# Kernel tuning notes

Hardware: AMD Instinct MI355X
Metric: run time of the kernel (lower is better)

The kernel has to match this reference:

```python
import jax, jax.numpy as jnp
import numpy as np

HIDDEN = 4096
N_HEADS = 32
N_KV_HEADS = 8
HEAD_DIM = HIDDEN // N_HEADS  # 128
N_REP = N_HEADS // N_KV_HEADS  # 4
ROPE_THETA = 10000.0
B, S = 2, 2048


def setup_inputs() -> dict:
    key = jax.random.key(0)
    ks = jax.random.split(key, 9)
    sc = 1.0 / np.sqrt(HIDDEN)
    query = jax.random.normal(ks[0], (B, S, HIDDEN), jnp.float32)
    key_t = jax.random.normal(ks[1], (B, S, HIDDEN), jnp.float32)
    value = jax.random.normal(ks[2], (B, S, HIDDEN), jnp.float32)
    position_ids = jnp.sort(jax.random.randint(ks[3], (B, S), 0, S), axis=-1)
    Wq = jax.random.normal(ks[4], (HIDDEN, N_HEADS * HEAD_DIM), jnp.float32) * sc
    Wk = jax.random.normal(ks[5], (HIDDEN, N_KV_HEADS * HEAD_DIM), jnp.float32) * sc
    Wv = jax.random.normal(ks[6], (HIDDEN, N_KV_HEADS * HEAD_DIM), jnp.float32) * sc
    Wo = jax.random.normal(ks[7], (N_HEADS * HEAD_DIM, HIDDEN), jnp.float32) * sc
    return {"query": query, "key": key_t, "value": value,
            "position_ids": position_ids,
            "Wq": Wq, "Wk": Wk, "Wv": Wv, "Wo": Wo}


def _rotate_half(x):
    x1, x2 = jnp.split(x, 2, axis=-1)
    return jnp.concatenate((-x2, x1), axis=-1)


def _rope_cos_sin(position_ids):
    # inv_freq: [head_dim/2]
    inv_freq = 1.0 / (ROPE_THETA ** (jnp.arange(0, HEAD_DIM, 2, dtype=jnp.float32) / HEAD_DIM))
    # freqs: [B, S, head_dim/2] via per-position lookup (equiv. to cache gather cos_cached[position_ids])
    freqs = position_ids[..., None].astype(jnp.float32) * inv_freq
    emb = jnp.concatenate((freqs, freqs), axis=-1)          # [B, S, head_dim]
    return jnp.cos(emb)[:, None, :, :], jnp.sin(emb)[:, None, :, :]  # [B,1,S,hd]


def reference(query, key, value, position_ids, Wq, Wk, Wv, Wo):
    nb, q_len, _ = query.shape
    # QKV projections (bias-free linear)
    q = jnp.einsum('bse,ef->bsf', query, Wq).reshape(nb, q_len, N_HEADS, HEAD_DIM).transpose(0, 2, 1, 3)
    k = jnp.einsum('bse,ef->bsf', key, Wk).reshape(nb, q_len, N_KV_HEADS, HEAD_DIM).transpose(0, 2, 1, 3)
    v = jnp.einsum('bse,ef->bsf', value, Wv).reshape(nb, q_len, N_KV_HEADS, HEAD_DIM).transpose(0, 2, 1, 3)
    # RoPE
    cos, sin = _rope_cos_sin(position_ids)
    q = q * cos + _rotate_half(q) * sin
    k = k * cos + _rotate_half(k) * sin
    # GQA repeat_kv: [B, kvH, S, d] -> [B, H, S, d]
    k = jnp.repeat(k, N_REP, axis=1)
    v = jnp.repeat(v, N_REP, axis=1)
    # scaled dot-product attention (flash-attn semantics, no padding mask)
    scale = 1.0 / jnp.sqrt(jnp.asarray(HEAD_DIM, q.dtype))
    scores = jnp.einsum('bhqd,bhkd->bhqk', q, k) * scale
    probs = jax.nn.softmax(scores, axis=-1)
    ctx = jnp.einsum('bhqk,bhkd->bhqd', probs, v)
    ctx = ctx.transpose(0, 2, 1, 3).reshape(nb, q_len, N_HEADS * HEAD_DIM)
    return jnp.einsum('bsf,fe->bse', ctx, Wo)
```

## Files before the change

### kernel.cpp

```cpp
#include <hip/hip_runtime.h>
#include <hip/hip_bf16.h>

typedef __attribute__((ext_vector_type(8))) short bf16x8;
typedef __attribute__((ext_vector_type(4))) float f32x4;
typedef __attribute__((ext_vector_type(16))) float f32x16;
typedef __attribute__((ext_vector_type(2))) float f32x2;
typedef __attribute__((ext_vector_type(2))) unsigned uint2x;

#define AS1(p) ((const __attribute__((address_space(1))) void*)(p))
#define AS3(p) ((__attribute__((address_space(3))) void*)(p))

__device__ inline unsigned cvtpk_bf16(float lo, float hi) {
  unsigned r;
  asm("v_cvt_pk_bf16_f32 %0, %1, %2" : "=v"(r) : "v"(lo), "v"(hi));
  return r;
}

__device__ inline uint2x plswap(unsigned a, unsigned b) {
  return __builtin_amdgcn_permlane32_swap(a, b, false, false);
}

__device__ inline f32x2 pkadd(f32x2 a, f32x2 b) {
  f32x2 d;
  asm("v_pk_add_f32 %0, %1, %2" : "=v"(d) : "v"(a), "v"(b));
  return d;
}
__device__ inline f32x2 pkmul(f32x2 a, f32x2 b) {
  f32x2 d;
  asm("v_pk_mul_f32 %0, %1, %2" : "=v"(d) : "v"(a), "v"(b));
  return d;
}


__global__ __launch_bounds__(256) void xconv_kv(const float* __restrict__ k_in,
                                                const float* __restrict__ v_in,
                                                __hip_bfloat16* __restrict__ kc,
                                                __hip_bfloat16* __restrict__ vc) {
  const float* in = blockIdx.y ? v_in : k_in;
  __hip_bfloat16* out = blockIdx.y ? vc : kc;
  size_t i = ((size_t)blockIdx.x * 256 + threadIdx.x) * 4;
  float4 v = *(const float4*)(in + i);
  union { __hip_bfloat16 h[4]; ushort4 u; } o;
  o.h[0] = __float2bfloat16(v.x);
  o.h[1] = __float2bfloat16(v.y);
  o.h[2] = __float2bfloat16(v.z);
  o.h[3] = __float2bfloat16(v.w);
  *(ushort4*)(out + i) = o.u;
}

__global__ __launch_bounds__(256) void xconv(const float* __restrict__ in,
                                             __hip_bfloat16* __restrict__ out) {
  size_t i = ((size_t)blockIdx.x * 256 + threadIdx.x) * 4;
  float4 v = *(const float4*)(in + i);
  union { __hip_bfloat16 h[4]; ushort4 u; } o;
  o.h[0] = __float2bfloat16(v.x);
  o.h[1] = __float2bfloat16(v.y);
  o.h[2] = __float2bfloat16(v.z);
  o.h[3] = __float2bfloat16(v.w);
  *(ushort4*)(out + i) = o.u;
}

__global__ __launch_bounds__(256) void wtransAll(const float* __restrict__ Wq,
                                                 const float* __restrict__ Wo,
                                                 const float* __restrict__ Wk,
                                                 const float* __restrict__ Wv,
                                                 __hip_bfloat16* __restrict__ WqT,
                                                 __hip_bfloat16* __restrict__ WoT,
                                                 __hip_bfloat16* __restrict__ WkT,
                                                 __hip_bfloat16* __restrict__ WvT) {
  const int z = blockIdx.z;
  const int N = (z < 2) ? 4096 : 1024;
  const int n0 = blockIdx.x << 5;
  if (n0 >= N) return;
  const float* W = (z == 0) ? Wq : (z == 1) ? Wo : (z == 2) ? Wk : Wv;
  __hip_bfloat16* WT = (z == 0) ? WqT : (z == 1) ? WoT : (z == 2) ? WkT : WvT;
  __shared__ float t[32][33];
  const int k0 = blockIdx.y << 5;
  const int tx = threadIdx.x, ty = threadIdx.y;
#pragma unroll
  for (int j = 0; j < 4; ++j)
    t[ty + j * 8][tx] = W[(size_t)(k0 + ty + j * 8) * N + n0 + tx];
  __syncthreads();
#pragma unroll
  for (int j = 0; j < 4; ++j)
    WT[(size_t)(n0 + ty + j * 8) * 4096 + k0 + tx] = __float2bfloat16(t[tx][ty + j * 8]);
}

__global__ __launch_bounds__(256) void rope(__hip_bfloat16* __restrict__ X,
                                            const int* __restrict__ pos,
                                            int hbits, float scale) {
  const int t = blockIdx.x * 256 + threadIdx.x;
  const int j = t & 63;
  const int rest = t >> 6;
  const int h = rest & ((1 << hbits) - 1);
  const int row = rest >> hbits;
  const float p = (float)pos[row];
  const float fr = p * exp2f((float)j * -0.2076205059304601f);
  float sn, cs;
  __sincosf(fr, &sn, &cs);
  const size_t base = (((size_t)row << hbits) + h) * 128 + j;
  const float x0 = __bfloat162float(X[base]);
  const float x1 = __bfloat162float(X[base + 64]);
  X[base]      = __float2bfloat16((x0 * cs - x1 * sn) * scale);
  X[base + 64] = __float2bfloat16((x1 * cs + x0 * sn) * scale);
}

__global__ __launch_bounds__(256) void gemm_kv(const __hip_bfloat16* __restrict__ Ak,
                                               const __hip_bfloat16* __restrict__ Av,
                                               const __hip_bfloat16* __restrict__ BkT,
                                               const __hip_bfloat16* __restrict__ BvT,
                                               __hip_bfloat16* __restrict__ Kp,
                                               __hip_bfloat16* __restrict__ VT) {
  __shared__ __align__(16) __hip_bfloat16 sh[17408];
  __hip_bfloat16* As = sh;
  __hip_bfloat16* Bs = sh + 8192;
  const int zz = blockIdx.z;
  const __hip_bfloat16* A  = zz ? Av : Ak;
  const __hip_bfloat16* BT = zz ? BvT : BkT;
  const int K = 4096, N = 1024;
  const int tid = threadIdx.x;
  const int lane = tid & 63, w = tid >> 6;
  const int m0 = blockIdx.y * 128, n0 = blockIdx.x * 128;
  const int wr = (w >> 1) * 64, wc = (w & 1) * 64;
  const int l15 = lane & 15, lg = lane >> 4;

  f32x4 acc[4][4] = {};
  const int srow = lane >> 3;
  const int scol = (lane & 7) * 8;

  for (int k0 = 0; k0 < K; k0 += 64) {
    __syncthreads();
#pragma unroll
    for (int i = 0; i < 4; ++i) {
      const int chunk = i * 4 + w;
      const int row = chunk * 8 + srow;
      __builtin_amdgcn_global_load_lds(AS1(A + (size_t)(m0 + row) * K + k0 + scol),
                                       AS3(As + chunk * 512), 16, 0, 0);
      __builtin_amdgcn_global_load_lds(AS1(BT + (size_t)(n0 + row) * K + k0 + scol),
                                       AS3(Bs + chunk * 512), 16, 0, 0);
    }
    __syncthreads();
#pragma unroll
    for (int kk = 0; kk < 2; ++kk) {
      bf16x8 af[4], bfr[4];
#pragma unroll
      for (int r = 0; r < 4; ++r) {
        af[r]  = *(const bf16x8*)(As + (wr + r * 16 + l15) * 64 + kk * 32 + lg * 8);
        bfr[r] = *(const bf16x8*)(Bs + (wc + r * 16 + l15) * 64 + kk * 32 + lg * 8);
      }
#pragma unroll
      for (int r = 0; r < 4; ++r)
#pragma unroll
        for (int c = 0; c < 4; ++c)
          acc[r][c] = __builtin_amdgcn_mfma_f32_16x16x32_bf16(af[r], bfr[c], acc[r][c], 0, 0, 0);
    }
  }

  if (zz == 0) {
#pragma unroll
    for (int r = 0; r < 4; ++r)
#pragma unroll
      for (int c = 0; c < 4; ++c)
#pragma unroll
        for (int i = 0; i < 4; ++i)
          Kp[(size_t)(m0 + wr + r * 16 + lg * 4 + i) * N + n0 + wc + c * 16 + l15] =
              __float2bfloat16(acc[r][c][i]);
  } else {
    __syncthreads();
    __hip_bfloat16* T = sh;
#pragma unroll
    for (int r = 0; r < 4; ++r)
#pragma unroll
      for (int c = 0; c < 4; ++c) {
        const int col = wc + c * 16 + l15;
        const int row = wr + r * 16 + lg * 4;
        union { __hip_bfloat16 h[4]; unsigned long long u; } pkv;
#pragma unroll
        for (int i = 0; i < 4; ++i) pkv.h[i] = __float2bfloat16(acc[r][c][i]);
        *(unsigned long long*)(T + col * 136 + row) = pkv.u;
      }
    __syncthreads();
    const int b = m0 >> 11, s0g = m0 & 2047, g = n0 >> 7;
    __hip_bfloat16* Vh = VT + (size_t)(b * 8 + g) * 128 * 2048;
    const int chunk = tid & 15;
#pragma unroll
    for (int it = 0; it < 8; ++it) {
      const int d = it * 16 + (tid >> 4);
      bf16x8 vv = *(const bf16x8*)(T + d * 136 + chunk * 8);
      *(bf16x8*)(Vh + (size_t)d * 2048 + s0g + chunk * 8) = vv;
    }
  }
}


__device__ inline int tile_off(int row, int k) {
  return (((row >> 4) << 1) + (k >> 5)) * 512 + (row & 15) * 32 +
         ((k & 31) ^ ((row & 8) << 1));
}

__device__ inline void stageA(const __hip_bfloat16* __restrict__ src, int ld, int row0,
                              int kt, int h, __hip_bfloat16* ldsT, int w, int lane) {
#pragma unroll
  for (int li = 0; li < 2; ++li) {
    const int t = li * 8 + w;
    const int grp = ((t >> 3) << 1) + h;
    const int srl = (t & 7) >> 1, sk = t & 1;
    const int rowbase = grp * 64 + srl * 16;
    __hip_bfloat16* dst = ldsT + ((((rowbase >> 4) << 1) + sk) << 9);
    const int r = lane >> 2;
    const int ku = (lane & 3) ^ ((r & 8) >> 2);
    __builtin_amdgcn_global_load_lds(
        AS1(src + (size_t)(row0 + rowbase + r) * ld + kt + (sk << 5) + (ku << 3)),
        AS3(dst), 16, 0, 0);
  }
}

__device__ inline void stageB(const __hip_bfloat16* __restrict__ src, int ld, int col0,
                              int kt, int h, __hip_bfloat16* ldsT, int w, int lane) {
#pragma unroll
  for (int li = 0; li < 2; ++li) {
    const int t = li * 8 + w;
    const int q = t >> 2;
    const int srl = (t >> 1) & 1, sk = t & 1;
    const int colbase = q * 64 + h * 32 + srl * 16;
    __hip_bfloat16* dst = ldsT + ((((colbase >> 4) << 1) + sk) << 9);
    const int r = lane >> 2;
    const int ku = (lane & 3) ^ ((r & 8) >> 2);
    __builtin_amdgcn_global_load_lds(
        AS1(src + (size_t)(col0 + colbase + r) * ld + kt + (sk << 5) + (ku << 3)),
        AS3(dst), 16, 0, 0);
  }
}

template <int OUT_F32>
__global__ __launch_bounds__(512, 1) void gemm256(const __hip_bfloat16* __restrict__ A,
                                                  const __hip_bfloat16* __restrict__ BT,
                                                  void* __restrict__ Cout,
                                                  int M, int N, int K) {
  __shared__ __align__(16) __hip_bfloat16 lds[2][2][16384];
  const int tid = threadIdx.x;
  const int lane = tid & 63, w = tid >> 6;
  const int l15 = lane & 15, lg = lane >> 4;
  const int wm = w >> 2, wn = w & 3;
  const int nbx = N >> 8;
  const int nwg = (M >> 8) * nbx;
  const int bid = blockIdx.x;
  const int swz = (bid & 7) * (nwg >> 3) + (bid >> 3);
  const int m0 = (swz / nbx) << 8, n0 = (swz % nbx) << 8;

  f32x4 acc[8][4] = {};
  const int NT = K >> 6;

  stageA(A, K, m0, 0, 0, &lds[0][0][0], w, lane);
  stageB(BT, K, n0, 0, 0, &lds[0][1][0], w, lane);
  stageA(A, K, m0, 0, 1, &lds[0][0][0], w, lane);
  stageB(BT, K, n0, 0, 1, &lds[0][1][0], w, lane);
  stageA(A, K, m0, 64, 0, &lds[1][0][0], w, lane);
  stageB(BT, K, n0, 64, 0, &lds[1][1][0], w, lane);
  asm volatile("s_waitcnt vmcnt(4)" ::: "memory");
  __builtin_amdgcn_s_barrier();

  for (int j = 0; j < NT; ++j) {
    const int buf = j & 1;
    const __hip_bfloat16* Ab = &lds[buf][0][0];
    const __hip_bfloat16* Bb = &lds[buf][1][0];
    __hip_bfloat16* An = &lds[buf ^ 1][0][0];
    __hip_bfloat16* Bn = &lds[buf ^ 1][1][0];
    __hip_bfloat16* Ac = &lds[buf][0][0];
    __hip_bfloat16* Bc = &lds[buf][1][0];
    const int kt1 = (j + 1) << 6, kt2 = (j + 2) << 6;
    const bool s1 = (j + 1) < NT, s2 = (j + 2) < NT;

    auto phase = [&](int rq, int cq, int sid) {
      bf16x8 af[2][4], bfr[2][2];
#pragma unroll
      for (int kk = 0; kk < 2; ++kk) {
#pragma unroll
        for (int rf = 0; rf < 4; ++rf)
          af[kk][rf] = *(const bf16x8*)(Ab +
              tile_off(wm * 128 + (rq * 4 + rf) * 16 + l15, kk * 32 + lg * 8));
#pragma unroll
        for (int cf = 0; cf < 2; ++cf)
          bfr[kk][cf] = *(const bf16x8*)(Bb +
              tile_off(wn * 64 + (cq * 2 + cf) * 16 + l15, kk * 32 + lg * 8));
      }
      if (sid == 0)      { if (s1) stageA(A, K, m0, kt1, 1, An, w, lane); }
      else if (sid == 1) { if (s1) stageB(BT, K, n0, kt1, 1, Bn, w, lane); }
      else if (sid == 2) { if (s2) stageA(A, K, m0, kt2, 0, Ac, w, lane); }
      else {
        if (s2) stageB(BT, K, n0, kt2, 0, Bc, w, lane);
        if (s2) asm volatile("s_waitcnt vmcnt(4)" ::: "memory");
        else    asm volatile("s_waitcnt vmcnt(0)" ::: "memory");
      }
      __builtin_amdgcn_s_barrier();
      asm volatile("s_waitcnt lgkmcnt(0)" ::: "memory");
      __builtin_amdgcn_sched_barrier(0);
      __builtin_amdgcn_s_setprio(1);
#pragma unroll
      for (int kk = 0; kk < 2; ++kk)
#pragma unroll
        for (int rf = 0; rf < 4; ++rf)
#pragma unroll
          for (int cf = 0; cf < 2; ++cf)
            acc[rq * 4 + rf][cq * 2 + cf] = __builtin_amdgcn_mfma_f32_16x16x32_bf16(
                af[kk][rf], bfr[kk][cf], acc[rq * 4 + rf][cq * 2 + cf], 0, 0, 0);
      __builtin_amdgcn_s_setprio(0);
      __builtin_amdgcn_s_barrier();
    };
    phase(0, 0, 0);
    phase(0, 1, 1);
    phase(1, 0, 2);
    phase(1, 1, 3);
  }

#pragma unroll
  for (int rf = 0; rf < 8; ++rf)
#pragma unroll
    for (int cf = 0; cf < 4; ++cf)
#pragma unroll
      for (int i = 0; i < 4; ++i) {
        const size_t row = (size_t)(m0 + wm * 128 + rf * 16 + lg * 4 + i);
        const size_t col = (size_t)(n0 + wn * 64 + cf * 16 + l15);
        if (OUT_F32)
          ((float*)Cout)[row * N + col] = acc[rf][cf][i];
        else
          ((__hip_bfloat16*)Cout)[row * N + col] = __float2bfloat16(acc[rf][cf][i]);
      }
}

__global__ __launch_bounds__(512) void attn(const __hip_bfloat16* __restrict__ Q,
                                            const __hip_bfloat16* __restrict__ Kp,
                                            const __hip_bfloat16* __restrict__ VT,
                                            const int* __restrict__ pos,
                                            __hip_bfloat16* __restrict__ ctx,
                                            float qs) {
  const int tid = threadIdx.x;
  const int lane = tid & 63, w = tid >> 6;
  const int l31 = lane & 31, hi = lane >> 5;
  const int qt = blockIdx.x, h = blockIdx.y, b = blockIdx.z;
  const int kvh = h >> 2;
  const int q0 = qt * 256 + w * 32;

  const __hip_bfloat16* Qh = Q + (size_t)(b * 2048) * 4096 + h * 128;
  const __hip_bfloat16* Kh = Kp + (size_t)(b * 2048) * 1024 + kvh * 128;
  const __hip_bfloat16* Vh = VT + (size_t)(b * 8 + kvh) * 128 * 2048;

  __shared__ __hip_bfloat16 Ks[2][64 * 128];
  __shared__ __hip_bfloat16 Vs[2][128 * 64];

  auto stage = [&](int buf, int s0) {
#pragma unroll
    for (int j = 0; j < 2; ++j) {
      const int idx = w * 64 + lane + j * 512;
      const int rK = idx >> 4, uK = idx & 15;
      __builtin_amdgcn_global_load_lds(
          AS1(Kh + (size_t)(s0 + rK) * 1024 + ((uK ^ (rK & 7)) << 3)),
          AS3(&Ks[buf][(w * 64 + j * 512) * 8]), 16, 0, 0);
      const int rV = idx >> 3, uV = idx & 7;
      __builtin_amdgcn_global_load_lds(
          AS1(Vh + (size_t)rV * 2048 + s0 + ((uV ^ (rV & 7)) << 3)),
          AS3(&Vs[buf][(w * 64 + j * 512) * 8]), 16, 0, 0);
    }
  };

  stage(0, 0);

  const int qrow = q0 + l31;
  const float pp = (float)pos[b * 2048 + qrow];
  bf16x8 qf[8];
  {
#pragma unroll
    for (int kd = 0; kd < 4; ++kd) {
      bf16x8 rlo = *(const bf16x8*)(Qh + (size_t)qrow * 4096 + kd * 16 + hi * 8);
      bf16x8 rhi = *(const bf16x8*)(Qh + (size_t)qrow * 4096 + (kd + 4) * 16 + hi * 8);
      bf16x8 olo, ohi;
#pragma unroll
      for (int e = 0; e < 8; ++e) {
        const int j = kd * 16 + hi * 8 + e;
        const float fr = pp * exp2f((float)j * -0.2076205059304601f);
        float sn, cs;
        __sincosf(fr, &sn, &cs);
        const float x0 = __uint_as_float(((unsigned)(unsigned short)rlo[e]) << 16);
        const float x1 = __uint_as_float(((unsigned)(unsigned short)rhi[e]) << 16);
        __hip_bfloat16 h0 = __float2bfloat16((x0 * cs - x1 * sn) * qs);
        __hip_bfloat16 h1 = __float2bfloat16((x1 * cs + x0 * sn) * qs);
        olo[e] = *(short*)&h0;
        ohi[e] = *(short*)&h1;
      }
      qf[kd] = olo;
      qf[kd + 4] = ohi;
    }
  }

  f32x16 o[4] = {};
  float m = -1e30f, lsum = 0.f;
  __syncthreads();

  auto tile = [&](int tt, int cur, bool pf) {
    if (pf) stage(cur ^ 1, (tt + 1) * 64);

    f32x16 p[2] = {};
    __builtin_amdgcn_s_setprio(1);
#pragma unroll
    for (int n = 0; n < 2; ++n)
#pragma unroll
      for (int kd = 0; kd < 8; ++kd) {
        const int row = n * 32 + l31;
        bf16x8 kf = *(const bf16x8*)(&Ks[cur][row * 128 + (((2 * kd + hi) ^ (row & 7)) << 3)]);
        p[n] = __builtin_amdgcn_mfma_f32_32x32x16_bf16(kf, qf[kd], p[n], 0, 0, 0);
      }
    __builtin_amdgcn_s_setprio(0);

    float t16[16];
#pragma unroll
    for (int e = 0; e < 16; ++e) t16[e] = fmaxf(p[0][e], p[1][e]);
    const float u0 = fmaxf(fmaxf(t16[0], t16[1]), t16[2]);
    const float u1 = fmaxf(fmaxf(t16[3], t16[4]), t16[5]);
    const float u2 = fmaxf(fmaxf(t16[6], t16[7]), t16[8]);
    const float u3 = fmaxf(fmaxf(t16[9], t16[10]), t16[11]);
    const float u4 = fmaxf(fmaxf(t16[12], t16[13]), t16[14]);
    float pmax = fmaxf(fmaxf(fmaxf(u0, u1), u2), fmaxf(fmaxf(u3, u4), t16[15]));
    {
      uint2x r = plswap(__float_as_uint(pmax), __float_as_uint(pmax));
      pmax = fmaxf(__uint_as_float(r[0]), __uint_as_float(r[1]));
    }
    if (!__all(pmax - m <= 8.0f)) {
      const float mnew = fmaxf(m, pmax);
      const float fac = exp2f(m - mnew);
      m = mnew;
      lsum *= fac;
      f32x2 f2; f2[0] = fac; f2[1] = fac;
#pragma unroll
      for (int dc = 0; dc < 4; ++dc)
#pragma unroll
        for (int i = 0; i < 8; ++i) {
          f32x2 a; a[0] = o[dc][2 * i]; a[1] = o[dc][2 * i + 1];
          a = pkmul(a, f2);
          o[dc][2 * i] = a[0]; o[dc][2 * i + 1] = a[1];
        }
    }
    f32x2 mneg; mneg[0] = -m; mneg[1] = -m;
#pragma unroll
    for (int n = 0; n < 2; ++n)
#pragma unroll
      for (int i = 0; i < 8; ++i) {
        f32x2 a; a[0] = p[n][2 * i]; a[1] = p[n][2 * i + 1];
        a = pkadd(a, mneg);
        p[n][2 * i] = exp2f(a[0]);
        p[n][2 * i + 1] = exp2f(a[1]);
      }
    f32x2 s[8];
#pragma unroll
    for (int i = 0; i < 8; ++i) {
      f32x2 a; a[0] = p[0][2 * i]; a[1] = p[0][2 * i + 1];
      f32x2 bb; bb[0] = p[1][2 * i]; bb[1] = p[1][2 * i + 1];
      s[i] = pkadd(a, bb);
    }
#pragma unroll
    for (int i = 0; i < 4; ++i) s[i] = pkadd(s[i], s[i + 4]);
    s[0] = pkadd(s[0], s[2]);
    s[1] = pkadd(s[1], s[3]);
    s[0] = pkadd(s[0], s[1]);
    float rs = s[0][0] + s[0][1];
    {
      uint2x r = plswap(__float_as_uint(rs), __float_as_uint(rs));
      rs = __uint_as_float(r[0]) + __uint_as_float(r[1]);
    }
    lsum += rs;

    __builtin_amdgcn_s_setprio(1);
#pragma unroll
    for (int n = 0; n < 2; ++n)
#pragma unroll
      for (int ks = 0; ks < 2; ++ks) {
        const int bse = ks * 8;
        unsigned a1 = cvtpk_bf16(p[n][bse + 0], p[n][bse + 1]);
        unsigned b1 = cvtpk_bf16(p[n][bse + 4], p[n][bse + 5]);
        unsigned a2 = cvtpk_bf16(p[n][bse + 2], p[n][bse + 3]);
        unsigned b2 = cvtpk_bf16(p[n][bse + 6], p[n][bse + 7]);
        uint2x s1 = plswap(a1, b1);
        uint2x s2 = plswap(a2, b2);
        union { unsigned u[4]; bf16x8 v; } pw = {{s1[0], s2[0], s1[1], s2[1]}};
        const int slot = n * 2 + ks;
#pragma unroll
        for (int dc = 0; dc < 4; ++dc) {
          const int row = dc * 32 + l31;
          bf16x8 vf = *(const bf16x8*)(&Vs[cur][row * 64 + (((2 * slot + hi) ^ (row & 7)) << 3)]);
          o[dc] = __builtin_amdgcn_mfma_f32_32x32x16_bf16(vf, pw.v, o[dc], 0, 0, 0);
        }
      }
    __builtin_amdgcn_s_setprio(0);
    __syncthreads();
  };

  for (int t2 = 0; t2 < 16; ++t2) {
    tile(2 * t2, 0, true);
    tile(2 * t2 + 1, 1, t2 < 15);
  }

  const float inv = 1.0f / lsum;
  const size_t rowbase = ((size_t)(b * 2048 + q0 + l31)) * 4096 + h * 128;
#pragma unroll
  for (int dc = 0; dc < 4; ++dc)
#pragma unroll
    for (int g = 0; g < 4; ++g) {
      union { unsigned short us[4]; ushort4 u4; } pk;
#pragma unroll
      for (int e = 0; e < 4; ++e) {
        __hip_bfloat16 hv = __float2bfloat16(o[dc][g * 4 + e] * inv);
        pk.us[e] = *(unsigned short*)&hv;
      }
      *(ushort4*)(ctx + rowbase + dc * 32 + g * 8 + hi * 4) = pk.u4;
    }
}


extern "C" void kernel_launch(void* const* d_in, const int* in_sizes, int n_in,
                              void* d_out, int out_size, void* d_ws, size_t ws_size,
                              hipStream_t stream) {
  const float* q_in = (const float*)d_in[0];
  const float* k_in = (const float*)d_in[1];
  const float* v_in = (const float*)d_in[2];
  const int* pos    = (const int*)d_in[3];
  const float* Wq   = (const float*)d_in[4];
  const float* Wk   = (const float*)d_in[5];
  const float* Wv   = (const float*)d_in[6];
  const float* Wo   = (const float*)d_in[7];

  char* ws = (char*)d_ws;
  __hip_bfloat16* xbuf = (__hip_bfloat16*)(ws);
  __hip_bfloat16* WqT  = (__hip_bfloat16*)(ws + 33554432);
  __hip_bfloat16* WkT  = (__hip_bfloat16*)(ws + 67108864);
  __hip_bfloat16* WvT  = (__hip_bfloat16*)(ws + 75497472);
  __hip_bfloat16* WoT  = (__hip_bfloat16*)(ws + 83886080);
  __hip_bfloat16* Qp   = (__hip_bfloat16*)(ws + 117440512);
  __hip_bfloat16* Kp   = (__hip_bfloat16*)(ws + 150994944);
  __hip_bfloat16* VTb  = (__hip_bfloat16*)(ws + 167772160);
  __hip_bfloat16* vconv = WqT;

  wtransAll<<<dim3(128, 128, 4), dim3(32, 8), 0, stream>>>(Wq, Wo, Wk, Wv,
                                                           WqT, WoT, WkT, WvT);
  xconv<<<16384, 256, 0, stream>>>(q_in, xbuf);
  gemm256<0><<<256, 512, 0, stream>>>(xbuf, WqT, Qp, 4096, 4096, 4096);
  xconv_kv<<<dim3(16384, 2), 256, 0, stream>>>(k_in, v_in, xbuf, vconv);
  gemm_kv<<<dim3(8, 32, 2), 256, 0, stream>>>(xbuf, vconv, WkT, WvT, Kp, VTb);
  rope<<<8192, 256, 0, stream>>>(Kp, pos, 3, 1.0f);
  attn<<<dim3(8, 32, 2), 512, 0, stream>>>(Qp, Kp, VTb, pos, xbuf,
                                           0.08838834764831845f * 1.4426950408889634f);
  gemm256<1><<<256, 512, 0, stream>>>(xbuf, WoT, d_out, 4096, 4096, 4096);
}
```

Before: 662.4 us.

## Rework weight transpose, KV GEMM pipeline, and attention V loads

The weight transpose now works on 64x64 tiles with float4 loads and packed bf16 stores. The K/V projection GEMM is replaced by a 512-thread, double-buffered, four-phase pipelined kernel with swizzled tile layout and a block-order swizzle, and V^T is written straight from registers. Attention stops staging V in LDS and reads V fragments directly from global memory. Packed-add/mul inline asm in the softmax is replaced by plain scalar code. Direct global V reads may add latency in the attention inner loop.

```diff
diff --git a/kernel.cpp b/kernel.cpp
--- a/kernel.cpp
+++ b/kernel.cpp
@@ -18,17 +18,6 @@
 
 __device__ inline uint2x plswap(unsigned a, unsigned b) {
   return __builtin_amdgcn_permlane32_swap(a, b, false, false);
-}
-
-__device__ inline f32x2 pkadd(f32x2 a, f32x2 b) {
-  f32x2 d;
-  asm("v_pk_add_f32 %0, %1, %2" : "=v"(d) : "v"(a), "v"(b));
-  return d;
-}
-__device__ inline f32x2 pkmul(f32x2 a, f32x2 b) {
-  f32x2 d;
-  asm("v_pk_mul_f32 %0, %1, %2" : "=v"(d) : "v"(a), "v"(b));
-  return d;
 }
 
 
@@ -70,20 +59,34 @@
                                                  __hip_bfloat16* __restrict__ WvT) {
   const int z = blockIdx.z;
   const int N = (z < 2) ? 4096 : 1024;
-  const int n0 = blockIdx.x << 5;
+  const int n0 = blockIdx.x << 6;
   if (n0 >= N) return;
   const float* W = (z == 0) ? Wq : (z == 1) ? Wo : (z == 2) ? Wk : Wv;
   __hip_bfloat16* WT = (z == 0) ? WqT : (z == 1) ? WoT : (z == 2) ? WkT : WvT;
-  __shared__ float t[32][33];
-  const int k0 = blockIdx.y << 5;
-  const int tx = threadIdx.x, ty = threadIdx.y;
-#pragma unroll
-  for (int j = 0; j < 4; ++j)
-    t[ty + j * 8][tx] = W[(size_t)(k0 + ty + j * 8) * N + n0 + tx];
+  __shared__ float t[64][68];
+  const int k0 = blockIdx.y << 6;
+  const int tx = threadIdx.x & 15, ty = threadIdx.x >> 4;
+#pragma unroll
+  for (int j = 0; j < 4; ++j) {
+    const int k = ty + j * 16;
+    float4 v = *(const float4*)(W + (size_t)(k0 + k) * N + n0 + tx * 4);
+    t[tx * 4 + 0][k] = v.x;
+    t[tx * 4 + 1][k] = v.y;
+    t[tx * 4 + 2][k] = v.z;
+    t[tx * 4 + 3][k] = v.w;
+  }
   __syncthreads();
 #pragma unroll
-  for (int j = 0; j < 4; ++j)
-    WT[(size_t)(n0 + ty + j * 8) * 4096 + k0 + tx] = __float2bfloat16(t[tx][ty + j * 8]);
+  for (int j = 0; j < 4; ++j) {
+    const int n = ty + j * 16;
+    float4 v = *(const float4*)(&t[n][tx * 4]);
+    union { __hip_bfloat16 h[4]; ushort4 u; } o;
+    o.h[0] = __float2bfloat16(v.x);
+    o.h[1] = __float2bfloat16(v.y);
+    o.h[2] = __float2bfloat16(v.z);
+    o.h[3] = __float2bfloat16(v.w);
+    *(ushort4*)(WT + (size_t)(n0 + n) * 4096 + k0 + tx * 4) = o.u;
+  }
 }
 
 __global__ __launch_bounds__(256) void rope(__hip_bfloat16* __restrict__ X,
@@ -105,93 +108,6 @@
   X[base + 64] = __float2bfloat16((x1 * cs + x0 * sn) * scale);
 }
 
-__global__ __launch_bounds__(256) void gemm_kv(const __hip_bfloat16* __restrict__ Ak,
-                                               const __hip_bfloat16* __restrict__ Av,
-                                               const __hip_bfloat16* __restrict__ BkT,
-                                               const __hip_bfloat16* __restrict__ BvT,
-                                               __hip_bfloat16* __restrict__ Kp,
-                                               __hip_bfloat16* __restrict__ VT) {
-  __shared__ __align__(16) __hip_bfloat16 sh[17408];
-  __hip_bfloat16* As = sh;
-  __hip_bfloat16* Bs = sh + 8192;
-  const int zz = blockIdx.z;
-  const __hip_bfloat16* A  = zz ? Av : Ak;
-  const __hip_bfloat16* BT = zz ? BvT : BkT;
-  const int K = 4096, N = 1024;
-  const int tid = threadIdx.x;
-  const int lane = tid & 63, w = tid >> 6;
-  const int m0 = blockIdx.y * 128, n0 = blockIdx.x * 128;
-  const int wr = (w >> 1) * 64, wc = (w & 1) * 64;
-  const int l15 = lane & 15, lg = lane >> 4;
-
-  f32x4 acc[4][4] = {};
-  const int srow = lane >> 3;
-  const int scol = (lane & 7) * 8;
-
-  for (int k0 = 0; k0 < K; k0 += 64) {
-    __syncthreads();
-#pragma unroll
-    for (int i = 0; i < 4; ++i) {
-      const int chunk = i * 4 + w;
-      const int row = chunk * 8 + srow;
-      __builtin_amdgcn_global_load_lds(AS1(A + (size_t)(m0 + row) * K + k0 + scol),
-                                       AS3(As + chunk * 512), 16, 0, 0);
-      __builtin_amdgcn_global_load_lds(AS1(BT + (size_t)(n0 + row) * K + k0 + scol),
-                                       AS3(Bs + chunk * 512), 16, 0, 0);
-    }
-    __syncthreads();
-#pragma unroll
-    for (int kk = 0; kk < 2; ++kk) {
-      bf16x8 af[4], bfr[4];
-#pragma unroll
-      for (int r = 0; r < 4; ++r) {
-        af[r]  = *(const bf16x8*)(As + (wr + r * 16 + l15) * 64 + kk * 32 + lg * 8);
-        bfr[r] = *(const bf16x8*)(Bs + (wc + r * 16 + l15) * 64 + kk * 32 + lg * 8);
-      }
-#pragma unroll
-      for (int r = 0; r < 4; ++r)
-#pragma unroll
-        for (int c = 0; c < 4; ++c)
-          acc[r][c] = __builtin_amdgcn_mfma_f32_16x16x32_bf16(af[r], bfr[c], acc[r][c], 0, 0, 0);
-    }
-  }
-
-  if (zz == 0) {
-#pragma unroll
-    for (int r = 0; r < 4; ++r)
-#pragma unroll
-      for (int c = 0; c < 4; ++c)
-#pragma unroll
-        for (int i = 0; i < 4; ++i)
-          Kp[(size_t)(m0 + wr + r * 16 + lg * 4 + i) * N + n0 + wc + c * 16 + l15] =
-              __float2bfloat16(acc[r][c][i]);
-  } else {
-    __syncthreads();
-    __hip_bfloat16* T = sh;
-#pragma unroll
-    for (int r = 0; r < 4; ++r)
-#pragma unroll
-      for (int c = 0; c < 4; ++c) {
-        const int col = wc + c * 16 + l15;
-        const int row = wr + r * 16 + lg * 4;
-        union { __hip_bfloat16 h[4]; unsigned long long u; } pkv;
-#pragma unroll
-        for (int i = 0; i < 4; ++i) pkv.h[i] = __float2bfloat16(acc[r][c][i]);
-        *(unsigned long long*)(T + col * 136 + row) = pkv.u;
-      }
-    __syncthreads();
-    const int b = m0 >> 11, s0g = m0 & 2047, g = n0 >> 7;
-    __hip_bfloat16* Vh = VT + (size_t)(b * 8 + g) * 128 * 2048;
-    const int chunk = tid & 15;
-#pragma unroll
-    for (int it = 0; it < 8; ++it) {
-      const int d = it * 16 + (tid >> 4);
-      bf16x8 vv = *(const bf16x8*)(T + d * 136 + chunk * 8);
-      *(bf16x8*)(Vh + (size_t)d * 2048 + s0g + chunk * 8) = vv;
-    }
-  }
-}
-
 
 __device__ inline int tile_off(int row, int k) {
   return (((row >> 4) << 1) + (k >> 5)) * 512 + (row & 15) * 32 +
@@ -328,6 +244,144 @@
       }
 }
 
+__global__ __launch_bounds__(512, 1) void gemm_kv8(const __hip_bfloat16* __restrict__ Ak,
+                                                   const __hip_bfloat16* __restrict__ Av,
+                                                   const __hip_bfloat16* __restrict__ BkT,
+                                                   const __hip_bfloat16* __restrict__ BvT,
+                                                   __hip_bfloat16* __restrict__ Kp,
+                                                   __hip_bfloat16* __restrict__ VT) {
+  __shared__ __align__(16) __hip_bfloat16 lds[2][24576];
+  const int zz = blockIdx.z;
+  const __hip_bfloat16* A  = zz ? Av : Ak;
+  const __hip_bfloat16* BT = zz ? BvT : BkT;
+  const int K = 4096;
+  const int tid = threadIdx.x;
+  const int lane = tid & 63, w = tid >> 6;
+  const int l15 = lane & 15, lg = lane >> 4;
+  const int wm = w >> 2, wn = w & 3;
+  const int bid = blockIdx.x;
+  const int swz = (bid & 7) * 16 + (bid >> 3);
+  const int m0 = (swz >> 2) << 7;
+  const int n0 = (swz & 3) << 8;
+
+  auto stgA = [&](int kt, int h, __hip_bfloat16* ldsA) {
+    const int r16 = 2 * h + ((w >> 2) << 2) + ((w >> 1) & 1);
+    const int sk = w & 1;
+    __hip_bfloat16* dst = ldsA + (((r16 << 1) + sk) << 9);
+    const int r = lane >> 2;
+    const int ku = (lane & 3) ^ ((r & 8) >> 2);
+    __builtin_amdgcn_global_load_lds(
+        AS1(A + (size_t)(m0 + r16 * 16 + r) * K + kt + (sk << 5) + (ku << 3)),
+        AS3(dst), 16, 0, 0);
+  };
+  auto stgB = [&](int kt, int h, __hip_bfloat16* ldsB) {
+#pragma unroll
+    for (int li = 0; li < 2; ++li) {
+      const int idx = li * 8 + w;
+      const int r16 = ((idx >> 2) << 2) + 2 * h + ((idx >> 1) & 1);
+      const int sk = idx & 1;
+      __hip_bfloat16* dst = ldsB + (((r16 << 1) + sk) << 9);
+      const int r = lane >> 2;
+      const int ku = (lane & 3) ^ ((r & 8) >> 2);
+      __builtin_amdgcn_global_load_lds(
+          AS1(BT + (size_t)(n0 + r16 * 16 + r) * K + kt + (sk << 5) + (ku << 3)),
+          AS3(dst), 16, 0, 0);
+    }
+  };
+
+  f32x4 acc[4][4] = {};
+  const int NT = K >> 6;
+
+  stgA(0, 0, &lds[0][0]);
+  stgB(0, 0, &lds[0][8192]);
+  stgA(0, 1, &lds[0][0]);
+  stgB(0, 1, &lds[0][8192]);
+  stgA(64, 0, &lds[1][0]);
+  stgB(64, 0, &lds[1][8192]);
+  asm volatile("s_waitcnt vmcnt(3)" ::: "memory");
+  __builtin_amdgcn_s_barrier();
+
+  for (int j = 0; j < NT; ++j) {
+    const int buf = j & 1;
+    const __hip_bfloat16* Ab = &lds[buf][0];
+    const __hip_bfloat16* Bb = &lds[buf][8192];
+    __hip_bfloat16* An = &lds[buf ^ 1][0];
+    __hip_bfloat16* Bn = &lds[buf ^ 1][8192];
+    __hip_bfloat16* Ac = &lds[buf][0];
+    __hip_bfloat16* Bc = &lds[buf][8192];
+    const int kt1 = (j + 1) << 6, kt2 = (j + 2) << 6;
+    const bool s1 = (j + 1) < NT, s2 = (j + 2) < NT;
+
+    auto phase = [&](int rq, int cq, int sid) {
+      bf16x8 af[2][2], bfr[2][2];
+#pragma unroll
+      for (int kk = 0; kk < 2; ++kk) {
+#pragma unroll
+        for (int rf = 0; rf < 2; ++rf)
+          af[kk][rf] = *(const bf16x8*)(Ab +
+              tile_off(wm * 64 + (rq * 2 + rf) * 16 + l15, kk * 32 + lg * 8));
+#pragma unroll
+        for (int cf = 0; cf < 2; ++cf)
+          bfr[kk][cf] = *(const bf16x8*)(Bb +
+              tile_off(wn * 64 + (cq * 2 + cf) * 16 + l15, kk * 32 + lg * 8));
+      }
+      if (sid == 0)      { if (s1) stgA(kt1, 1, An); }
+      else if (sid == 1) { if (s1) stgB(kt1, 1, Bn); }
+      else if (sid == 2) { if (s2) stgA(kt2, 0, Ac); }
+      else {
+        if (s2) stgB(kt2, 0, Bc);
+        if (s2) asm volatile("s_waitcnt vmcnt(3)" ::: "memory");
+        else    asm volatile("s_waitcnt vmcnt(0)" ::: "memory");
+      }
+      __builtin_amdgcn_s_barrier();
+      asm volatile("s_waitcnt lgkmcnt(0)" ::: "memory");
+      __builtin_amdgcn_sched_barrier(0);
+      __builtin_amdgcn_s_setprio(1);
+#pragma unroll
+      for (int kk = 0; kk < 2; ++kk)
+#pragma unroll
+        for (int rf = 0; rf < 2; ++rf)
+#pragma unroll
+          for (int cf = 0; cf < 2; ++cf)
+            acc[rq * 2 + rf][cq * 2 + cf] = __builtin_amdgcn_mfma_f32_16x16x32_bf16(
+                af[kk][rf], bfr[kk][cf], acc[rq * 2 + rf][cq * 2 + cf], 0, 0, 0);
+      __builtin_amdgcn_s_setprio(0);
+      __builtin_amdgcn_s_barrier();
+    };
+    phase(0, 0, 0);
+    phase(0, 1, 1);
+    phase(1, 0, 2);
+    phase(1, 1, 3);
+  }
+
+  if (zz == 0) {
+#pragma unroll
+    for (int rf = 0; rf < 4; ++rf)
+#pragma unroll
+      for (int cf = 0; cf < 4; ++cf)
+#pragma unroll
+        for (int i = 0; i < 4; ++i) {
+          const size_t row = (size_t)(m0 + wm * 64 + rf * 16 + lg * 4 + i);
+          const size_t col = (size_t)(n0 + wn * 64 + cf * 16 + l15);
+          Kp[row * 1024 + col] = __float2bfloat16(acc[rf][cf][i]);
+        }
+  } else {
+    const int b = m0 >> 11, s0g = m0 & 2047;
+#pragma unroll
+    for (int rf = 0; rf < 4; ++rf)
+#pragma unroll
+      for (int cf = 0; cf < 4; ++cf) {
+        const int d = n0 + wn * 64 + cf * 16 + l15;
+        const int g = d >> 7, dl = d & 127;
+        const int srow = s0g + wm * 64 + rf * 16 + lg * 4;
+        union { __hip_bfloat16 h[4]; unsigned long long u; } pkv;
+#pragma unroll
+        for (int i = 0; i < 4; ++i) pkv.h[i] = __float2bfloat16(acc[rf][cf][i]);
+        *(unsigned long long*)(VT + ((size_t)(b * 8 + g) * 128 + dl) * 2048 + srow) = pkv.u;
+      }
+  }
+}
+
 __global__ __launch_bounds__(512) void attn(const __hip_bfloat16* __restrict__ Q,
                                             const __hip_bfloat16* __restrict__ Kp,
                                             const __hip_bfloat16* __restrict__ VT,
@@ -346,7 +400,6 @@
   const __hip_bfloat16* Vh = VT + (size_t)(b * 8 + kvh) * 128 * 2048;
 
   __shared__ __hip_bfloat16 Ks[2][64 * 128];
-  __shared__ __hip_bfloat16 Vs[2][128 * 64];
 
   auto stage = [&](int buf, int s0) {
 #pragma unroll
@@ -356,10 +409,6 @@
       __builtin_amdgcn_global_load_lds(
           AS1(Kh + (size_t)(s0 + rK) * 1024 + ((uK ^ (rK & 7)) << 3)),
           AS3(&Ks[buf][(w * 64 + j * 512) * 8]), 16, 0, 0);
-      const int rV = idx >> 3, uV = idx & 7;
-      __builtin_amdgcn_global_load_lds(
-          AS1(Vh + (size_t)rV * 2048 + s0 + ((uV ^ (rV & 7)) << 3)),
-          AS3(&Vs[buf][(w * 64 + j * 512) * 8]), 16, 0, 0);
     }
   };
 
@@ -429,39 +478,23 @@
       const float fac = exp2f(m - mnew);
       m = mnew;
       lsum *= fac;
-      f32x2 f2; f2[0] = fac; f2[1] = fac;
 #pragma unroll
       for (int dc = 0; dc < 4; ++dc)
 #pragma unroll
-        for (int i = 0; i < 8; ++i) {
-          f32x2 a; a[0] = o[dc][2 * i]; a[1] = o[dc][2 * i + 1];
-          a = pkmul(a, f2);
-          o[dc][2 * i] = a[0]; o[dc][2 * i + 1] = a[1];
-        }
-    }
-    f32x2 mneg; mneg[0] = -m; mneg[1] = -m;
+        for (int e = 0; e < 16; ++e) o[dc][e] *= fac;
+    }
 #pragma unroll
     for (int n = 0; n < 2; ++n)
 #pragma unroll
-      for (int i = 0; i < 8; ++i) {
-        f32x2 a; a[0] = p[n][2 * i]; a[1] = p[n][2 * i + 1];
-        a = pkadd(a, mneg);
-        p[n][2 * i] = exp2f(a[0]);
-        p[n][2 * i + 1] = exp2f(a[1]);
-      }
-    f32x2 s[8];
-#pragma unroll
-    for (int i = 0; i < 8; ++i) {
-      f32x2 a; a[0] = p[0][2 * i]; a[1] = p[0][2 * i + 1];
-      f32x2 bb; bb[0] = p[1][2 * i]; bb[1] = p[1][2 * i + 1];
-      s[i] = pkadd(a, bb);
-    }
-#pragma unroll
-    for (int i = 0; i < 4; ++i) s[i] = pkadd(s[i], s[i + 4]);
-    s[0] = pkadd(s[0], s[2]);
-    s[1] = pkadd(s[1], s[3]);
-    s[0] = pkadd(s[0], s[1]);
-    float rs = s[0][0] + s[0][1];
+      for (int e = 0; e < 16; ++e) p[n][e] = exp2f(p[n][e] - m);
+    float s16[16];
+#pragma unroll
+    for (int e = 0; e < 16; ++e) s16[e] = p[0][e] + p[1][e];
+#pragma unroll
+    for (int e = 0; e < 8; ++e) s16[e] = s16[e] + s16[e + 8];
+#pragma unroll
+    for (int e = 0; e < 4; ++e) s16[e] = s16[e] + s16[e + 4];
+    float rs = (s16[0] + s16[1]) + (s16[2] + s16[3]);
     {
       uint2x r = plswap(__float_as_uint(rs), __float_as_uint(rs));
       rs = __uint_as_float(r[0]) + __uint_as_float(r[1]);
@@ -484,8 +517,8 @@
         const int slot = n * 2 + ks;
 #pragma unroll
         for (int dc = 0; dc < 4; ++dc) {
-          const int row = dc * 32 + l31;
-          bf16x8 vf = *(const bf16x8*)(&Vs[cur][row * 64 + (((2 * slot + hi) ^ (row & 7)) << 3)]);
+          bf16x8 vf = *(const bf16x8*)(Vh + (size_t)(dc * 32 + l31) * 2048 +
+                                       tt * 64 + ((2 * slot + hi) << 3));
           o[dc] = __builtin_amdgcn_mfma_f32_32x32x16_bf16(vf, pw.v, o[dc], 0, 0, 0);
         }
       }
@@ -538,12 +571,11 @@
   __hip_bfloat16* VTb  = (__hip_bfloat16*)(ws + 167772160);
   __hip_bfloat16* vconv = WqT;
 
-  wtransAll<<<dim3(128, 128, 4), dim3(32, 8), 0, stream>>>(Wq, Wo, Wk, Wv,
-                                                           WqT, WoT, WkT, WvT);
+  wtransAll<<<dim3(64, 64, 4), 256, 0, stream>>>(Wq, Wo, Wk, Wv, WqT, WoT, WkT, WvT);
   xconv<<<16384, 256, 0, stream>>>(q_in, xbuf);
   gemm256<0><<<256, 512, 0, stream>>>(xbuf, WqT, Qp, 4096, 4096, 4096);
   xconv_kv<<<dim3(16384, 2), 256, 0, stream>>>(k_in, v_in, xbuf, vconv);
-  gemm_kv<<<dim3(8, 32, 2), 256, 0, stream>>>(xbuf, vconv, WkT, WvT, Kp, VTb);
+  gemm_kv8<<<dim3(128, 1, 2), 512, 0, stream>>>(xbuf, vconv, WkT, WvT, Kp, VTb);
   rope<<<8192, 256, 0, stream>>>(Kp, pos, 3, 1.0f);
   attn<<<dim3(8, 32, 2), 512, 0, stream>>>(Qp, Kp, VTb, pos, xbuf,
                                            0.08838834764831845f * 1.4426950408889634f);
```

After: 800.8 us. +20.9%, slower.
